# Optimization experiments

Measured on AMD Instinct MI355X. Metric: run time of the kernel, lower is better.

## Reference

```python
import jax, jax.numpy as jnp
import numpy as np

NUM_HEAD = 8


def setup_inputs() -> dict:
    key = jax.random.key(0)
    ks = jax.random.split(key, 9)
    B, T, Hz, N, H, Tc = 8, 48, 24, 1024, 512, 64
    return {
        "encoder_hidden": jax.random.normal(ks[0], (B, T, N, H), dtype=jnp.float32),
        "x_time": jax.random.normal(ks[1], (B, T, Tc), dtype=jnp.float32),
        "target_time": jax.random.normal(ks[2], (B, Hz, Tc), dtype=jnp.float32),
        "Wq": jax.random.normal(ks[3], (Tc, H), dtype=jnp.float32) * (Tc ** -0.5),
        "bq": jax.random.normal(ks[4], (H,), dtype=jnp.float32) * 0.02,
        "Wk": jax.random.normal(ks[5], (Tc, H), dtype=jnp.float32) * (Tc ** -0.5),
        "bk": jax.random.normal(ks[6], (H,), dtype=jnp.float32) * 0.02,
        "Wv": jax.random.normal(ks[7], (H, H), dtype=jnp.float32) * (H ** -0.5),
        "bv": jax.random.normal(ks[8], (H,), dtype=jnp.float32) * 0.02,
    }


def reference(encoder_hidden, x_time, target_time, Wq, bq, Wk, bk, Wv, bv):
    # encoder_hidden: [B, T, N, H]; x_time: [B, T, Tc]; target_time: [B, Hz, Tc]
    B, T, N, H = encoder_hidden.shape
    nh = NUM_HEAD
    d = H // nh
    Hz = target_time.shape[1]
    # Linear projections; split/cat over heads == reshape last dim to [nh, d]
    q = (target_time @ Wq + bq).reshape(B, Hz, nh, d)      # [B, Hz, nh, d]
    k = (x_time @ Wk + bk).reshape(B, T, nh, d)            # [B, T, nh, d]
    v = (encoder_hidden @ Wv + bv).reshape(B, T, N, nh, d)  # [B, T, N, nh, d]
    # Attention over time, shared across nodes
    scores = jnp.einsum('bihd,bjhd->bhij', q, k) / (d ** 0.5)  # [B, nh, Hz, T]
    attn = jax.nn.softmax(scores, axis=-1)
    # Broadcast attention across the node dimension
    X = jnp.einsum('bhij,bjnhd->binhd', attn, v)           # [B, Hz, N, nh, d]
    return X.reshape(B, Hz, N, H)                           # [B, Hz, N, H]
```

## Files before the change

kernel.cpp:

```cpp
#include <hip/hip_runtime.h>
#include <hip/hip_bf16.h>

#define Bb 8
#define Tt 48
#define HZ 24
#define Nn 1024
#define Hh 512
#define NHEAD 8

typedef short short8 __attribute__((ext_vector_type(8)));
typedef short bf16x4 __attribute__((ext_vector_type(4)));
typedef float f32x4 __attribute__((ext_vector_type(4)));

__device__ __forceinline__ ushort f2bf(float f) {
  uint u = __builtin_bit_cast(uint, f);
  u += 0x7FFFu + ((u >> 16) & 1u);
  return (ushort)(u >> 16);
}

__device__ __forceinline__ f32x4 mfma16(bf16x4 a, bf16x4 b, f32x4 c) {
#if __has_builtin(__builtin_amdgcn_mfma_f32_16x16x16bf16_1k)
  return __builtin_amdgcn_mfma_f32_16x16x16bf16_1k(a, b, c, 0, 0, 0);
#elif __has_builtin(__builtin_amdgcn_mfma_f32_16x16x16_bf16)
  return __builtin_amdgcn_mfma_f32_16x16x16_bf16(a, b, c, 0, 0, 0);
#else
  f32x4 d;
  asm volatile("v_mfma_f32_16x16x16_bf16 %0, %1, %2, %3\n\ts_nop 7\n\ts_nop 4"
               : "=v"(d) : "v"(a), "v"(b), "v"(c));
  return d;
#endif
}

__global__ void wvt2_kernel(const float* __restrict__ Wv, ushort* __restrict__ W2) {
  int t = blockIdx.x * 256 + threadIdx.x;
  int e = t & 7;
  int lane = (t >> 3) & 63;
  int f = (t >> 9) & 3;
  int kb = (t >> 11) & 7;
  int w = (t >> 14) & 3;
  int ch = t >> 16;
  int ki = f >> 1, nn = f & 1;
  int row = ch * 128 + w * 32 + nn * 16 + (lane & 15);
  int col = kb * 64 + ki * 32 + ((lane >> 4) << 3) + e;
  W2[t] = f2bf(Wv[col * 512 + row]);
}

__global__ void attn_kernel(const float* __restrict__ xt, const float* __restrict__ tt,
                            const float* __restrict__ Wq, const float* __restrict__ bq,
                            const float* __restrict__ Wk, const float* __restrict__ bk,
                            ushort* __restrict__ attnp) {
  __shared__ float qs[24][65];
  __shared__ float ks_[48][65];
  __shared__ float sc[24][49];
  int bh = blockIdx.x;
  int b = bh >> 3, h = bh & 7;
  int t = threadIdx.x;
  for (int e = t; e < 24 * 64; e += 256) {
    int i = e >> 6, dd = e & 63;
    float s = bq[h * 64 + dd];
    const float* r = tt + (b * 24 + i) * 64;
    #pragma unroll 8
    for (int c = 0; c < 64; ++c) s += r[c] * Wq[c * 512 + h * 64 + dd];
    qs[i][dd] = s;
  }
  for (int e = t; e < 48 * 64; e += 256) {
    int j = e >> 6, dd = e & 63;
    float s = bk[h * 64 + dd];
    const float* r = xt + (b * 48 + j) * 64;
    #pragma unroll 8
    for (int c = 0; c < 64; ++c) s += r[c] * Wk[c * 512 + h * 64 + dd];
    ks_[j][dd] = s;
  }
  __syncthreads();
  for (int e = t; e < 24 * 48; e += 256) {
    int i = e / 48, j = e - i * 48;
    float s = 0.f;
    #pragma unroll 8
    for (int dd = 0; dd < 64; ++dd) s += qs[i][dd] * ks_[j][dd];
    sc[i][j] = s * 0.125f;
  }
  __syncthreads();
  if (t < 32) {
    int i = t;
    ushort* orow = attnp + ((size_t)bh * 32 + i) * 64;
    if (i < 24) {
      float mx = -1e30f;
      for (int j = 0; j < 48; ++j) mx = fmaxf(mx, sc[i][j]);
      float sum = 0.f;
      for (int j = 0; j < 48; ++j) { float e = expf(sc[i][j] - mx); sc[i][j] = e; sum += e; }
      float inv = 1.f / sum;
      for (int j = 0; j < 48; ++j) orow[j] = f2bf(sc[i][j] * inv);
      for (int j = 48; j < 64; ++j) orow[j] = 0;
    } else {
      for (int j = 0; j < 64; ++j) orow[j] = 0;
    }
  }
}

#define A_TILE 49152

__global__ __launch_bounds__(512, 1) void main_kernel(
    const float* __restrict__ EH, const ushort* __restrict__ W2,
    const ushort* __restrict__ attnp, const float* __restrict__ bv,
    float* __restrict__ out) {
  __shared__ __align__(128) char smem[98304];
  int bid = blockIdx.x;
  int b = bid >> 9, np = bid & 511;
  int t = threadIdx.x;
  int lane = t & 63, w = t >> 6;
  int g = w >> 2, w4 = w & 3;
  int rowl = lane & 15;
  int colb = (lane >> 4) << 3;
  int colb16 = (lane >> 4) << 2;
  const char* atile = smem + g * A_TILE;

  float bvr[4][2];
  #pragma unroll
  for (int c = 0; c < 4; ++c)
    #pragma unroll
    for (int nn = 0; nn < 2; ++nn)
      bvr[c][nn] = bv[c * 128 + w4 * 32 + nn * 16 + rowl];

  const ushort* wbase = W2 + (size_t)w4 * 16384 + lane * 8;

  short8 b0[4], b1[4], b2[4];
  #pragma unroll
  for (int f = 0; f < 4; ++f) b0[f] = *(const short8*)(wbase + f * 512);
  #pragma unroll
  for (int f = 0; f < 4; ++f) b1[f] = *(const short8*)(wbase + 2048 + f * 512);
  #pragma unroll
  for (int f = 0; f < 4; ++f) b2[f] = *(const short8*)(wbase + 4096 + f * 512);

  {
    int tt = t & 255, gs = t >> 8;
    const float* ehb = EH + (((size_t)b * Tt) * Nn + (np * 2 + gs)) * Hh;
    char* dst = smem + gs * A_TILE;
    #pragma unroll 8
    for (int it = 0; it < 24; ++it) {
      int f = it * 256 + tt;
      int j = f >> 7, c4 = f & 127;
      float4 v = *(const float4*)(ehb + (size_t)j * (Nn * Hh) + c4 * 4);
      uint2 p;
      p.x = (uint)f2bf(v.x) | ((uint)f2bf(v.y) << 16);
      p.y = (uint)f2bf(v.z) | ((uint)f2bf(v.w) << 16);
      int off = (j << 10) + (c4 << 3);
      off ^= (j & 7) << 4;
      *(uint2*)(dst + off) = p;
    }
  }
  __syncthreads();

  f32x4 acc[3][2] = {};
  #pragma unroll
  for (int ck = 0; ck < 32; ++ck) {
    const int kb = ck & 7;
    short8 bnext[4];
    if (ck < 29) {
      const int ck3 = ck + 3;
      const ushort* wp3 = wbase + (size_t)((ck3 >> 3) * 4) * 16384 + (ck3 & 7) * 2048;
      #pragma unroll
      for (int f = 0; f < 4; ++f) bnext[f] = *(const short8*)(wp3 + f * 512);
    }
    short8 af[2][3];
    #pragma unroll
    for (int ki = 0; ki < 2; ++ki) {
      int kc = kb * 64 + ki * 32 + colb;
      #pragma unroll
      for (int m = 0; m < 3; ++m) {
        int j = m * 16 + rowl;
        int off = (j << 10) + (kc << 1);
        off ^= (j & 7) << 4;
        af[ki][m] = *(const short8*)(atile + off);
      }
    }
    __builtin_amdgcn_s_setprio(1);
    #pragma unroll
    for (int m = 0; m < 3; ++m) {
      acc[m][0] = __builtin_amdgcn_mfma_f32_16x16x32_bf16(af[0][m], b0[0], acc[m][0], 0, 0, 0);
      acc[m][1] = __builtin_amdgcn_mfma_f32_16x16x32_bf16(af[0][m], b0[1], acc[m][1], 0, 0, 0);
    }
    #pragma unroll
    for (int m = 0; m < 3; ++m) {
      acc[m][0] = __builtin_amdgcn_mfma_f32_16x16x32_bf16(af[1][m], b0[2], acc[m][0], 0, 0, 0);
      acc[m][1] = __builtin_amdgcn_mfma_f32_16x16x32_bf16(af[1][m], b0[3], acc[m][1], 0, 0, 0);
    }
    __builtin_amdgcn_s_setprio(0);
    #pragma unroll
    for (int f = 0; f < 4; ++f) { b0[f] = b1[f]; b1[f] = b2[f]; }
    if (ck < 29) {
      #pragma unroll
      for (int f = 0; f < 4; ++f) b2[f] = bnext[f];
    }

    if (kb == 7) {
      const int ch = ck >> 3;
      int h = 2 * ch + (w4 >> 1);
      const ushort* arow = attnp + ((size_t)(b * 8 + h) * 32) * 64;
      int n = np * 2 + g;
      f32x4 x[2][2] = {};
      #pragma unroll
      for (int m = 0; m < 3; ++m) {
        bf16x4 pa[2];
        #pragma unroll
        for (int itl = 0; itl < 2; ++itl)
          pa[itl] = *(const bf16x4*)(arow + (itl * 16 + rowl) * 64 + m * 16 + colb16);
        #pragma unroll
        for (int nn = 0; nn < 2; ++nn) {
          bf16x4 vbq;
          vbq[0] = (short)f2bf(acc[m][nn][0]);
          vbq[1] = (short)f2bf(acc[m][nn][1]);
          vbq[2] = (short)f2bf(acc[m][nn][2]);
          vbq[3] = (short)f2bf(acc[m][nn][3]);
          x[0][nn] = mfma16(pa[0], vbq, x[0][nn]);
          x[1][nn] = mfma16(pa[1], vbq, x[1][nn]);
        }
      }
      #pragma unroll
      for (int itl = 0; itl < 2; ++itl) {
        int ib = itl * 16 + ((lane >> 4) << 2);
        #pragma unroll
        for (int nn = 0; nn < 2; ++nn) {
          int hd = ch * 128 + w4 * 32 + nn * 16 + rowl;
          float bvv = bvr[ch][nn];
          #pragma unroll
          for (int r = 0; r < 4; ++r) {
            int i = ib + r;
            if (i < 24)
              out[(((size_t)b * HZ + i) * Nn + n) * Hh + hd] = x[itl][nn][r] + bvv;
          }
        }
      }
      #pragma unroll
      for (int m = 0; m < 3; ++m)
        #pragma unroll
        for (int nn = 0; nn < 2; ++nn)
          acc[m][nn] = f32x4{0.f, 0.f, 0.f, 0.f};
    }
  }
}

extern "C" void kernel_launch(void* const* d_in, const int* in_sizes, int n_in,
                              void* d_out, int out_size, void* d_ws, size_t ws_size,
                              hipStream_t stream) {
  (void)in_sizes; (void)n_in; (void)out_size; (void)ws_size;
  const float* EH = (const float*)d_in[0];
  const float* xt = (const float*)d_in[1];
  const float* tt = (const float*)d_in[2];
  const float* Wq = (const float*)d_in[3];
  const float* bq = (const float*)d_in[4];
  const float* Wk = (const float*)d_in[5];
  const float* bk = (const float*)d_in[6];
  const float* Wv = (const float*)d_in[7];
  const float* bv = (const float*)d_in[8];
  float* out = (float*)d_out;
  ushort* W2 = (ushort*)d_ws;
  ushort* attnp = (ushort*)((char*)d_ws + 512 * 1024);

  wvt2_kernel<<<1024, 256, 0, stream>>>(Wv, W2);
  attn_kernel<<<64, 256, 0, stream>>>(xt, tt, Wq, bq, Wk, bk, attnp);
  main_kernel<<<4096, 512, 0, stream>>>(EH, W2, attnp, bv, out);
}
```

Before: 507.8 us.

## Reorder GEMM loop to load A fragments once per k-block across all chunks

Swaps the loop nest so each k-block's A fragments are read from LDS once and reused across all four 128-column output chunks. The accumulators grow to cover the full 512-wide output. Wv is re-laid out with k-block outermost to match the new streaming order, and the attention/epilogue step moves after the GEMM. Launch bounds are raised to 2 blocks per SM, which with 96KB LDS per block and the larger accumulator set risks register spills or no real gain in occupancy.

```diff
diff --git a/kernel.cpp b/kernel.cpp
--- a/kernel.cpp
+++ b/kernel.cpp
@@ -36,9 +36,9 @@
   int e = t & 7;
   int lane = (t >> 3) & 63;
   int f = (t >> 9) & 3;
-  int kb = (t >> 11) & 7;
-  int w = (t >> 14) & 3;
-  int ch = t >> 16;
+  int ch = (t >> 11) & 3;
+  int w = (t >> 13) & 3;
+  int kb = t >> 15;
   int ki = f >> 1, nn = f & 1;
   int row = ch * 128 + w * 32 + nn * 16 + (lane & 15);
   int col = kb * 64 + ki * 32 + ((lane >> 4) << 3) + e;
@@ -99,7 +99,7 @@
 
 #define A_TILE 49152
 
-__global__ __launch_bounds__(512, 1) void main_kernel(
+__global__ __launch_bounds__(512, 2) void main_kernel(
     const float* __restrict__ EH, const ushort* __restrict__ W2,
     const ushort* __restrict__ attnp, const float* __restrict__ bv,
     float* __restrict__ out) {
@@ -114,22 +114,16 @@
   int colb16 = (lane >> 4) << 2;
   const char* atile = smem + g * A_TILE;
 
-  float bvr[4][2];
-  #pragma unroll
-  for (int c = 0; c < 4; ++c)
-    #pragma unroll
-    for (int nn = 0; nn < 2; ++nn)
-      bvr[c][nn] = bv[c * 128 + w4 * 32 + nn * 16 + rowl];
-
-  const ushort* wbase = W2 + (size_t)w4 * 16384 + lane * 8;
+  const ushort* wbase = W2 + (size_t)w4 * 8192 + lane * 8;
+  #define WPTR(s) (wbase + (size_t)((s) >> 2) * 32768 + ((s) & 3) * 2048)
 
   short8 b0[4], b1[4], b2[4];
   #pragma unroll
-  for (int f = 0; f < 4; ++f) b0[f] = *(const short8*)(wbase + f * 512);
-  #pragma unroll
-  for (int f = 0; f < 4; ++f) b1[f] = *(const short8*)(wbase + 2048 + f * 512);
-  #pragma unroll
-  for (int f = 0; f < 4; ++f) b2[f] = *(const short8*)(wbase + 4096 + f * 512);
+  for (int f = 0; f < 4; ++f) b0[f] = *(const short8*)(WPTR(0) + f * 512);
+  #pragma unroll
+  for (int f = 0; f < 4; ++f) b1[f] = *(const short8*)(WPTR(1) + f * 512);
+  #pragma unroll
+  for (int f = 0; f < 4; ++f) b2[f] = *(const short8*)(WPTR(2) + f * 512);
 
   {
     int tt = t & 255, gs = t >> 8;
@@ -150,17 +144,16 @@
   }
   __syncthreads();
 
-  f32x4 acc[3][2] = {};
-  #pragma unroll
-  for (int ck = 0; ck < 32; ++ck) {
-    const int kb = ck & 7;
-    short8 bnext[4];
-    if (ck < 29) {
-      const int ck3 = ck + 3;
-      const ushort* wp3 = wbase + (size_t)((ck3 >> 3) * 4) * 16384 + (ck3 & 7) * 2048;
-      #pragma unroll
-      for (int f = 0; f < 4; ++f) bnext[f] = *(const short8*)(wp3 + f * 512);
-    }
+  float bvr[4][2];
+  #pragma unroll
+  for (int c = 0; c < 4; ++c)
+    #pragma unroll
+    for (int nn = 0; nn < 2; ++nn)
+      bvr[c][nn] = bv[c * 128 + w4 * 32 + nn * 16 + rowl];
+
+  f32x4 acc[4][3][2] = {};
+  #pragma unroll
+  for (int kb = 0; kb < 8; ++kb) {
     short8 af[2][3];
     #pragma unroll
     for (int ki = 0; ki < 2; ++ki) {
@@ -173,68 +166,71 @@
         af[ki][m] = *(const short8*)(atile + off);
       }
     }
-    __builtin_amdgcn_s_setprio(1);
+    #pragma unroll
+    for (int ch = 0; ch < 4; ++ch) {
+      const int s = kb * 4 + ch;
+      short8 bnext[4];
+      if (s < 29) {
+        const ushort* wp = WPTR(s + 3);
+        #pragma unroll
+        for (int f = 0; f < 4; ++f) bnext[f] = *(const short8*)(wp + f * 512);
+      }
+      #pragma unroll
+      for (int m = 0; m < 3; ++m) {
+        acc[ch][m][0] = __builtin_amdgcn_mfma_f32_16x16x32_bf16(af[0][m], b0[0], acc[ch][m][0], 0, 0, 0);
+        acc[ch][m][1] = __builtin_amdgcn_mfma_f32_16x16x32_bf16(af[0][m], b0[1], acc[ch][m][1], 0, 0, 0);
+      }
+      #pragma unroll
+      for (int m = 0; m < 3; ++m) {
+        acc[ch][m][0] = __builtin_amdgcn_mfma_f32_16x16x32_bf16(af[1][m], b0[2], acc[ch][m][0], 0, 0, 0);
+        acc[ch][m][1] = __builtin_amdgcn_mfma_f32_16x16x32_bf16(af[1][m], b0[3], acc[ch][m][1], 0, 0, 0);
+      }
+      #pragma unroll
+      for (int f = 0; f < 4; ++f) { b0[f] = b1[f]; b1[f] = b2[f]; }
+      if (s < 29) {
+        #pragma unroll
+        for (int f = 0; f < 4; ++f) b2[f] = bnext[f];
+      }
+    }
+  }
+
+  int n = np * 2 + g;
+  #pragma unroll
+  for (int ch = 0; ch < 4; ++ch) {
+    int h = 2 * ch + (w4 >> 1);
+    const ushort* arow = attnp + ((size_t)(b * 8 + h) * 32) * 64;
+    f32x4 x[2][2] = {};
     #pragma unroll
     for (int m = 0; m < 3; ++m) {
-      acc[m][0] = __builtin_amdgcn_mfma_f32_16x16x32_bf16(af[0][m], b0[0], acc[m][0], 0, 0, 0);
-      acc[m][1] = __builtin_amdgcn_mfma_f32_16x16x32_bf16(af[0][m], b0[1], acc[m][1], 0, 0, 0);
-    }
-    #pragma unroll
-    for (int m = 0; m < 3; ++m) {
-      acc[m][0] = __builtin_amdgcn_mfma_f32_16x16x32_bf16(af[1][m], b0[2], acc[m][0], 0, 0, 0);
-      acc[m][1] = __builtin_amdgcn_mfma_f32_16x16x32_bf16(af[1][m], b0[3], acc[m][1], 0, 0, 0);
-    }
-    __builtin_amdgcn_s_setprio(0);
-    #pragma unroll
-    for (int f = 0; f < 4; ++f) { b0[f] = b1[f]; b1[f] = b2[f]; }
-    if (ck < 29) {
-      #pragma unroll
-      for (int f = 0; f < 4; ++f) b2[f] = bnext[f];
-    }
-
-    if (kb == 7) {
-      const int ch = ck >> 3;
-      int h = 2 * ch + (w4 >> 1);
-      const ushort* arow = attnp + ((size_t)(b * 8 + h) * 32) * 64;
-      int n = np * 2 + g;
-      f32x4 x[2][2] = {};
-      #pragma unroll
-      for (int m = 0; m < 3; ++m) {
-        bf16x4 pa[2];
+      bf16x4 pa[2];
+      #pragma unroll
+      for (int itl = 0; itl < 2; ++itl)
+        pa[itl] = *(const bf16x4*)(arow + (itl * 16 + rowl) * 64 + m * 16 + colb16);
+      #pragma unroll
+      for (int nn = 0; nn < 2; ++nn) {
+        bf16x4 vbq;
+        vbq[0] = (short)f2bf(acc[ch][m][nn][0]);
+        vbq[1] = (short)f2bf(acc[ch][m][nn][1]);
+        vbq[2] = (short)f2bf(acc[ch][m][nn][2]);
+        vbq[3] = (short)f2bf(acc[ch][m][nn][3]);
+        x[0][nn] = mfma16(pa[0], vbq, x[0][nn]);
+        x[1][nn] = mfma16(pa[1], vbq, x[1][nn]);
+      }
+    }
+    #pragma unroll
+    for (int itl = 0; itl < 2; ++itl) {
+      int ib = itl * 16 + ((lane >> 4) << 2);
+      #pragma unroll
+      for (int nn = 0; nn < 2; ++nn) {
+        int hd = ch * 128 + w4 * 32 + nn * 16 + rowl;
+        float bvv = bvr[ch][nn];
         #pragma unroll
-        for (int itl = 0; itl < 2; ++itl)
-          pa[itl] = *(const bf16x4*)(arow + (itl * 16 + rowl) * 64 + m * 16 + colb16);
-        #pragma unroll
-        for (int nn = 0; nn < 2; ++nn) {
-          bf16x4 vbq;
-          vbq[0] = (short)f2bf(acc[m][nn][0]);
-          vbq[1] = (short)f2bf(acc[m][nn][1]);
-          vbq[2] = (short)f2bf(acc[m][nn][2]);
-          vbq[3] = (short)f2bf(acc[m][nn][3]);
-          x[0][nn] = mfma16(pa[0], vbq, x[0][nn]);
-          x[1][nn] = mfma16(pa[1], vbq, x[1][nn]);
+        for (int r = 0; r < 4; ++r) {
+          int i = ib + r;
+          if (i < 24)
+            out[(((size_t)b * HZ + i) * Nn + n) * Hh + hd] = x[itl][nn][r] + bvv;
         }
       }
-      #pragma unroll
-      for (int itl = 0; itl < 2; ++itl) {
-        int ib = itl * 16 + ((lane >> 4) << 2);
-        #pragma unroll
-        for (int nn = 0; nn < 2; ++nn) {
-          int hd = ch * 128 + w4 * 32 + nn * 16 + rowl;
-          float bvv = bvr[ch][nn];
-          #pragma unroll
-          for (int r = 0; r < 4; ++r) {
-            int i = ib + r;
-            if (i < 24)
-              out[(((size_t)b * HZ + i) * Nn + n) * Hh + hd] = x[itl][nn][r] + bvv;
-          }
-        }
-      }
-      #pragma unroll
-      for (int m = 0; m < 3; ++m)
-        #pragma unroll
-        for (int nn = 0; nn < 2; ++nn)
-          acc[m][nn] = f32x4{0.f, 0.f, 0.f, 0.f};
     }
   }
 }
```

Result: slower. 573.2 us (+12.9%).

## Make main kernel persistent over 32 nodes with double-buffered EH prefetch

Applied to the files above, without the earlier changes.

The main kernel moves from 4096 blocks handling two nodes each to 256 blocks that each loop over 32 consecutive (b,n) nodes. The next node's encoder_hidden slice is prefetched into registers while the current one is computed, then written into a second shared-memory buffer. Each wave now owns 64 output columns (one head) across the full K range, and the Wv layout is permuted to match, streaming Wv tiles two steps ahead. The aim is to hide global-load latency behind MFMA work and to amortise launch and prologue costs. In exchange it raises register pressure (prefetch buffers plus wider accumulators) and uses only 256 blocks, which may underfill the GPU.

```diff
diff --git a/kernel.cpp b/kernel.cpp
--- a/kernel.cpp
+++ b/kernel.cpp
@@ -35,12 +35,11 @@
   int t = blockIdx.x * 256 + threadIdx.x;
   int e = t & 7;
   int lane = (t >> 3) & 63;
-  int f = (t >> 9) & 3;
-  int kb = (t >> 11) & 7;
-  int w = (t >> 14) & 3;
-  int ch = t >> 16;
-  int ki = f >> 1, nn = f & 1;
-  int row = ch * 128 + w * 32 + nn * 16 + (lane & 15);
+  int f = (t >> 9) & 7;
+  int w8 = (t >> 12) & 7;
+  int kb = t >> 15;
+  int ki = f >> 2, nn = f & 3;
+  int row = w8 * 64 + nn * 16 + (lane & 15);
   int col = kb * 64 + ki * 32 + ((lane >> 4) << 3) + e;
   W2[t] = f2bf(Wv[col * 512 + row]);
 }
@@ -104,100 +103,100 @@
     const ushort* __restrict__ attnp, const float* __restrict__ bv,
     float* __restrict__ out) {
   __shared__ __align__(128) char smem[98304];
-  int bid = blockIdx.x;
-  int b = bid >> 9, np = bid & 511;
   int t = threadIdx.x;
   int lane = t & 63, w = t >> 6;
-  int g = w >> 2, w4 = w & 3;
   int rowl = lane & 15;
   int colb = (lane >> 4) << 3;
   int colb16 = (lane >> 4) << 2;
-  const char* atile = smem + g * A_TILE;
-
-  float bvr[4][2];
+  int gn0 = blockIdx.x * 32;
+  int sj = t >> 7, sc4 = t & 127;
+
+  float bvr[4];
   #pragma unroll
-  for (int c = 0; c < 4; ++c)
+  for (int nn = 0; nn < 4; ++nn) bvr[nn] = bv[w * 64 + nn * 16 + rowl];
+
+  #define WPTR(kbw) (W2 + (size_t)(kbw) * 32768 + w * 4096 + lane * 8)
+
+  {
+    int b = gn0 >> 10, n = gn0 & 1023;
+    const float* ehb = EH + (((size_t)b * Tt) * Nn + n) * Hh;
     #pragma unroll
-    for (int nn = 0; nn < 2; ++nn)
-      bvr[c][nn] = bv[c * 128 + w4 * 32 + nn * 16 + rowl];
-
-  const ushort* wbase = W2 + (size_t)w4 * 16384 + lane * 8;
-
-  short8 b0[4], b1[4], b2[4];
-  #pragma unroll
-  for (int f = 0; f < 4; ++f) b0[f] = *(const short8*)(wbase + f * 512);
-  #pragma unroll
-  for (int f = 0; f < 4; ++f) b1[f] = *(const short8*)(wbase + 2048 + f * 512);
-  #pragma unroll
-  for (int f = 0; f < 4; ++f) b2[f] = *(const short8*)(wbase + 4096 + f * 512);
-
-  {
-    int tt = t & 255, gs = t >> 8;
-    const float* ehb = EH + (((size_t)b * Tt) * Nn + (np * 2 + gs)) * Hh;
-    char* dst = smem + gs * A_TILE;
-    #pragma unroll 8
-    for (int it = 0; it < 24; ++it) {
-      int f = it * 256 + tt;
+    for (int s = 0; s < 12; ++s) {
+      int f = s * 512 + t;
       int j = f >> 7, c4 = f & 127;
       float4 v = *(const float4*)(ehb + (size_t)j * (Nn * Hh) + c4 * 4);
       uint2 p;
       p.x = (uint)f2bf(v.x) | ((uint)f2bf(v.y) << 16);
       p.y = (uint)f2bf(v.z) | ((uint)f2bf(v.w) << 16);
-      int off = (j << 10) + (c4 << 3);
-      off ^= (j & 7) << 4;
-      *(uint2*)(dst + off) = p;
-    }
-  }
+      int off = ((j << 10) + (c4 << 3)) ^ ((j & 7) << 4);
+      *(uint2*)(smem + off) = p;
+    }
+  }
+  short8 bq0[8], bq1[8];
+  #pragma unroll
+  for (int f = 0; f < 8; ++f) bq0[f] = *(const short8*)(WPTR(0) + f * 512);
+  #pragma unroll
+  for (int f = 0; f < 8; ++f) bq1[f] = *(const short8*)(WPTR(1) + f * 512);
   __syncthreads();
 
-  f32x4 acc[3][2] = {};
-  #pragma unroll
-  for (int ck = 0; ck < 32; ++ck) {
-    const int kb = ck & 7;
-    short8 bnext[4];
-    if (ck < 29) {
-      const int ck3 = ck + 3;
-      const ushort* wp3 = wbase + (size_t)((ck3 >> 3) * 4) * 16384 + (ck3 & 7) * 2048;
-      #pragma unroll
-      for (int f = 0; f < 4; ++f) bnext[f] = *(const short8*)(wp3 + f * 512);
-    }
-    short8 af[2][3];
+  int cur = 0;
+  f32x4 acc[3][4] = {};
+  for (int it = 0; it < 32; ++it) {
+    int gn = gn0 + it;
+    int b = gn >> 10, n = gn & 1023;
+    const char* atile = smem + cur * A_TILE;
+
+    float4 ldv[12];
+    if (it < 31) {
+      int gn1 = gn + 1;
+      int b1 = gn1 >> 10, n1 = gn1 & 1023;
+      const float* ehb = EH + (((size_t)b1 * Tt) * Nn + n1) * Hh;
+      #pragma unroll
+      for (int s = 0; s < 12; ++s) {
+        int f = s * 512 + t;
+        int j = f >> 7, c4 = f & 127;
+        ldv[s] = *(const float4*)(ehb + (size_t)j * (Nn * Hh) + c4 * 4);
+      }
+    }
+
     #pragma unroll
-    for (int ki = 0; ki < 2; ++ki) {
-      int kc = kb * 64 + ki * 32 + colb;
-      #pragma unroll
-      for (int m = 0; m < 3; ++m) {
-        int j = m * 16 + rowl;
-        int off = (j << 10) + (kc << 1);
-        off ^= (j & 7) << 4;
-        af[ki][m] = *(const short8*)(atile + off);
-      }
-    }
-    __builtin_amdgcn_s_setprio(1);
-    #pragma unroll
-    for (int m = 0; m < 3; ++m) {
-      acc[m][0] = __builtin_amdgcn_mfma_f32_16x16x32_bf16(af[0][m], b0[0], acc[m][0], 0, 0, 0);
-      acc[m][1] = __builtin_amdgcn_mfma_f32_16x16x32_bf16(af[0][m], b0[1], acc[m][1], 0, 0, 0);
-    }
-    #pragma unroll
-    for (int m = 0; m < 3; ++m) {
-      acc[m][0] = __builtin_amdgcn_mfma_f32_16x16x32_bf16(af[1][m], b0[2], acc[m][0], 0, 0, 0);
-      acc[m][1] = __builtin_amdgcn_mfma_f32_16x16x32_bf16(af[1][m], b0[3], acc[m][1], 0, 0, 0);
-    }
-    __builtin_amdgcn_s_setprio(0);
-    #pragma unroll
-    for (int f = 0; f < 4; ++f) { b0[f] = b1[f]; b1[f] = b2[f]; }
-    if (ck < 29) {
-      #pragma unroll
-      for (int f = 0; f < 4; ++f) b2[f] = bnext[f];
-    }
-
-    if (kb == 7) {
-      const int ch = ck >> 3;
-      int h = 2 * ch + (w4 >> 1);
-      const ushort* arow = attnp + ((size_t)(b * 8 + h) * 32) * 64;
-      int n = np * 2 + g;
-      f32x4 x[2][2] = {};
+    for (int kb = 0; kb < 8; ++kb) {
+      short8 bn[8];
+      {
+        const ushort* wp = WPTR((kb + 2) & 7);
+        #pragma unroll
+        for (int f = 0; f < 8; ++f) bn[f] = *(const short8*)(wp + f * 512);
+      }
+      short8 af[2][3];
+      #pragma unroll
+      for (int ki = 0; ki < 2; ++ki) {
+        int kc = kb * 64 + ki * 32 + colb;
+        #pragma unroll
+        for (int m = 0; m < 3; ++m) {
+          int j = m * 16 + rowl;
+          int off = ((j << 10) + (kc << 1)) ^ ((j & 7) << 4);
+          af[ki][m] = *(const short8*)(atile + off);
+        }
+      }
+      __builtin_amdgcn_s_setprio(1);
+      #pragma unroll
+      for (int m = 0; m < 3; ++m)
+        #pragma unroll
+        for (int nn = 0; nn < 4; ++nn)
+          acc[m][nn] = __builtin_amdgcn_mfma_f32_16x16x32_bf16(af[0][m], bq0[nn], acc[m][nn], 0, 0, 0);
+      #pragma unroll
+      for (int m = 0; m < 3; ++m)
+        #pragma unroll
+        for (int nn = 0; nn < 4; ++nn)
+          acc[m][nn] = __builtin_amdgcn_mfma_f32_16x16x32_bf16(af[1][m], bq0[4 + nn], acc[m][nn], 0, 0, 0);
+      __builtin_amdgcn_s_setprio(0);
+      #pragma unroll
+      for (int f = 0; f < 8; ++f) { bq0[f] = bq1[f]; bq1[f] = bn[f]; }
+    }
+
+    {
+      const ushort* arow = attnp + ((size_t)(b * 8 + w) * 32) * 64;
+      f32x4 x[2][4] = {};
       #pragma unroll
       for (int m = 0; m < 3; ++m) {
         bf16x4 pa[2];
@@ -205,7 +204,7 @@
         for (int itl = 0; itl < 2; ++itl)
           pa[itl] = *(const bf16x4*)(arow + (itl * 16 + rowl) * 64 + m * 16 + colb16);
         #pragma unroll
-        for (int nn = 0; nn < 2; ++nn) {
+        for (int nn = 0; nn < 4; ++nn) {
           bf16x4 vbq;
           vbq[0] = (short)f2bf(acc[m][nn][0]);
           vbq[1] = (short)f2bf(acc[m][nn][1]);
@@ -219,23 +218,38 @@
       for (int itl = 0; itl < 2; ++itl) {
         int ib = itl * 16 + ((lane >> 4) << 2);
         #pragma unroll
-        for (int nn = 0; nn < 2; ++nn) {
-          int hd = ch * 128 + w4 * 32 + nn * 16 + rowl;
-          float bvv = bvr[ch][nn];
+        for (int nn = 0; nn < 4; ++nn) {
+          int hd = w * 64 + nn * 16 + rowl;
           #pragma unroll
           for (int r = 0; r < 4; ++r) {
             int i = ib + r;
             if (i < 24)
-              out[(((size_t)b * HZ + i) * Nn + n) * Hh + hd] = x[itl][nn][r] + bvv;
+              out[(((size_t)b * HZ + i) * Nn + n) * Hh + hd] = x[itl][nn][r] + bvr[nn];
           }
         }
       }
       #pragma unroll
       for (int m = 0; m < 3; ++m)
         #pragma unroll
-        for (int nn = 0; nn < 2; ++nn)
+        for (int nn = 0; nn < 4; ++nn)
           acc[m][nn] = f32x4{0.f, 0.f, 0.f, 0.f};
     }
+
+    if (it < 31) {
+      char* dst = smem + (cur ^ 1) * A_TILE;
+      #pragma unroll
+      for (int s = 0; s < 12; ++s) {
+        int f = s * 512 + t;
+        int j = f >> 7, c4 = f & 127;
+        uint2 p;
+        p.x = (uint)f2bf(ldv[s].x) | ((uint)f2bf(ldv[s].y) << 16);
+        p.y = (uint)f2bf(ldv[s].z) | ((uint)f2bf(ldv[s].w) << 16);
+        int off = ((j << 10) + (c4 << 3)) ^ ((j & 7) << 4);
+        *(uint2*)(dst + off) = p;
+      }
+    }
+    __syncthreads();
+    cur ^= 1;
   }
 }
 
@@ -258,5 +272,5 @@
 
   wvt2_kernel<<<1024, 256, 0, stream>>>(Wv, W2);
   attn_kernel<<<64, 256, 0, stream>>>(xt, tt, Wq, bq, Wk, bk, attnp);
-  main_kernel<<<4096, 512, 0, stream>>>(EH, W2, attnp, bv, out);
-}
+  main_kernel<<<256, 512, 0, stream>>>(EH, W2, attnp, bv, out);
+}
```

New measurement: 1.354 ms. 167% more time.
